# Kernel optimization log

Measured on AMD Instinct MI355X. Metric: run time of the kernel, lower is better.

Reference implementation:

```python
import jax, jax.numpy as jnp
import numpy as np

B, L, D_MODEL, H, D_K, D_V, C = 4, 2048, 512, 8, 64, 64, 5
LN_EPS = 1e-5


def setup_inputs() -> dict:
    key = jax.random.key(0)
    ks = jax.random.split(key, 9)
    u_k = min(int(C * np.log(L)), L)  # 38
    s = 1.0 / np.sqrt(D_MODEL)
    return {
        "input_Q": jax.random.normal(ks[0], (B, L, D_MODEL), jnp.float32),
        "input_K": jax.random.normal(ks[1], (B, L, D_MODEL), jnp.float32),
        "input_V": jax.random.normal(ks[2], (B, L, D_MODEL), jnp.float32),
        "W_Q": jax.random.normal(ks[3], (D_MODEL, H * D_K), jnp.float32) * s,
        "W_K": jax.random.normal(ks[4], (D_MODEL, H * D_K), jnp.float32) * s,
        "W_V": jax.random.normal(ks[5], (D_MODEL, H * D_V), jnp.float32) * s,
        "W_fc": jax.random.normal(ks[6], (H * D_V, D_MODEL), jnp.float32) * (1.0 / np.sqrt(H * D_V)),
        "ln_gamma": jnp.ones((D_MODEL,), jnp.float32),
        "ln_beta": jnp.zeros((D_MODEL,), jnp.float32),
        "index_sample": jax.random.randint(ks[7], (L, u_k), 0, L, jnp.int32),
    }


def reference(input_Q, input_K, input_V, W_Q, W_K, W_V, W_fc, ln_gamma, ln_beta, index_sample):
    Bb, L_Q, _ = input_Q.shape
    L_K = input_K.shape[1]
    u_q = min(int(C * np.log(L_Q)), L_Q)  # n_top queries kept

    # projections -> (B, H, L, d)
    Q = (input_Q @ W_Q).reshape(Bb, L_Q, H, D_K).transpose(0, 2, 1, 3)
    K = (input_K @ W_K).reshape(Bb, L_K, H, D_K).transpose(0, 2, 1, 3)
    V = (input_V @ W_V).reshape(Bb, L_K, H, D_V).transpose(0, 2, 1, 3)

    # sampled QK scores: gather u_k random keys per query position
    K_sample = K[:, :, index_sample, :]                      # (B,H,L_Q,u_k,d_k)
    QK_sample = jnp.einsum('bhqe,bhqke->bhqk', Q, K_sample)  # (B,H,L_Q,u_k)

    # sparsity measure M = max - mean, top-u_q queries
    M = QK_sample.max(axis=-1) - QK_sample.mean(axis=-1)     # (B,H,L_Q)
    _, idx = jax.lax.top_k(M, u_q)                           # (B,H,u_q)

    # attention only for selected queries
    Q_sel = jnp.take_along_axis(Q, idx[..., None], axis=2)   # (B,H,u_q,d_k)
    scores = jnp.einsum('bhue,bhke->bhuk', Q_sel, K) / np.sqrt(D_K)
    attn = jax.nn.softmax(scores, axis=-1)
    values = jnp.einsum('bhuk,bhkd->bhud', attn, V)          # (B,H,u_q,d_v)

    # initial context = mean of V (attn_mask is None), scatter selected rows
    context = jnp.broadcast_to(V.mean(axis=2, keepdims=True), (Bb, H, L_Q, D_V))
    bb = jnp.arange(Bb)[:, None, None]
    hh = jnp.arange(H)[None, :, None]
    context = context.at[bb, hh, idx].set(values)

    context = context.transpose(0, 2, 1, 3).reshape(Bb, L_Q, H * D_V)
    out = context @ W_fc                                     # dropout p=0.0

    y = out + input_Q
    mu = y.mean(axis=-1, keepdims=True)
    var = jnp.mean(jnp.square(y - mu), axis=-1, keepdims=True)
    y = (y - mu) / jnp.sqrt(var + LN_EPS) * ln_gamma + ln_beta
    return y, idx
```

## Files before the change

kernel.cpp:

```cpp
#include <hip/hip_runtime.h>
#include <hip/hip_bf16.h>

#define NB 4
#define NL 2048
#define NH 8
#define NDM 512
#define ND 64
#define KSPLIT 16
#define KTILE 32
#define QB 8

typedef __attribute__((ext_vector_type(8))) short short8b;
typedef __attribute__((ext_vector_type(4))) float f32x4;

__global__ void wconv(const float* __restrict__ W, unsigned short* __restrict__ WT) {
  const int g = blockIdx.x * 256 + threadIdx.x;
  const int k = g >> 9, c = g & 511;
  __hip_bfloat16 hb = __float2bfloat16(W[(size_t)k * 512 + c]);
  WT[(size_t)c * 512 + k] = *reinterpret_cast<unsigned short*>(&hb);
}

__global__ void vmean_colmean(const float* __restrict__ inV, float* __restrict__ parts) {
  const int b = blockIdx.x, seg = blockIdx.y, t = threadIdx.x;
  const float* p = inV + ((size_t)b * NL + seg * 32) * NDM;
  float s0 = 0.f, s1 = 0.f;
  for (int r = 0; r < 32; ++r) {
    s0 += p[(size_t)r * NDM + t];
    s1 += p[(size_t)r * NDM + 256 + t];
  }
  parts[((size_t)b * 64 + seg) * NDM + t] = s0;
  parts[((size_t)b * 64 + seg) * NDM + 256 + t] = s1;
}
__global__ void vmean_gemm(const float* __restrict__ parts, const float* __restrict__ Wv,
                           float* __restrict__ Vm) {
  __shared__ float cm[512];
  const int b = blockIdx.x, t = threadIdx.x;
  float a0 = 0.f, a1 = 0.f;
  for (int g = 0; g < 64; ++g) {
    a0 += parts[((size_t)b * 64 + g) * NDM + t];
    a1 += parts[((size_t)b * 64 + g) * NDM + 256 + t];
  }
  cm[t] = a0 * (1.f / 2048.f);
  cm[t + 256] = a1 * (1.f / 2048.f);
  __syncthreads();
  const int c0 = blockIdx.y * 256 + t;
  float acc = 0.f;
  for (int k = 0; k < 512; ++k) acc += cm[k] * Wv[(size_t)k * NDM + c0];
  Vm[b * 512 + c0] = acc;
}

__global__ __launch_bounds__(256, 4) void proj3(
    const float* __restrict__ AQ, const float* __restrict__ AK,
    const float* __restrict__ wQm, const float* __restrict__ wKm,
    int gh0, float* __restrict__ Qc, float* __restrict__ Kc) {
  __shared__ float As_[32 * 132];
  __shared__ float Ws_[32 * 68];
  const int tid = threadIdx.x;
  const int bm = blockIdx.x;
  const int hl = blockIdx.y;
  const int mat = blockIdx.z;
  const int bh = gh0 + hl;
  const int b = bh >> 3, h = bh & 7;
  const float* A = (mat == 0) ? AQ : AK;
  const float* W = (mat == 0) ? wQm : wKm;
  float* D = (mat == 0) ? Qc : Kc;
  const float* Ab = A + (size_t)b * NL * NDM;
  const int colbase = h * 64;
  const int tm = tid >> 4, tn = tid & 15;
  float acc[8][4] = {};
  for (int k0 = 0; k0 < 512; k0 += 32) {
#pragma unroll
    for (int i = 0; i < 4; ++i) {
      int s = tid + i * 256;
      int r = s >> 3, c4 = (s & 7) * 4;
      float4 v = *reinterpret_cast<const float4*>(Ab + (size_t)(bm * 128 + r) * 512 + k0 + c4);
      As_[(c4 + 0) * 132 + r] = v.x;
      As_[(c4 + 1) * 132 + r] = v.y;
      As_[(c4 + 2) * 132 + r] = v.z;
      As_[(c4 + 3) * 132 + r] = v.w;
    }
#pragma unroll
    for (int i = 0; i < 2; ++i) {
      int s = tid + i * 256;
      int r = s >> 4, c4 = (s & 15) * 4;
      *reinterpret_cast<float4*>(&Ws_[r * 68 + c4]) =
          *reinterpret_cast<const float4*>(W + (size_t)(k0 + r) * 512 + colbase + c4);
    }
    __syncthreads();
#pragma unroll
    for (int kk = 0; kk < 32; ++kk) {
      float4 a0 = *reinterpret_cast<const float4*>(&As_[kk * 132 + tm * 4]);
      float4 a1 = *reinterpret_cast<const float4*>(&As_[kk * 132 + 64 + tm * 4]);
      float4 w  = *reinterpret_cast<const float4*>(&Ws_[kk * 68 + tn * 4]);
      float a[8] = {a0.x, a0.y, a0.z, a0.w, a1.x, a1.y, a1.z, a1.w};
      float wv[4] = {w.x, w.y, w.z, w.w};
#pragma unroll
      for (int ii = 0; ii < 8; ++ii)
#pragma unroll
        for (int jj = 0; jj < 4; ++jj) acc[ii][jj] += a[ii] * wv[jj];
    }
    __syncthreads();
  }
#pragma unroll
  for (int ii = 0; ii < 8; ++ii) {
    int row = bm * 128 + ((ii < 4) ? (tm * 4 + ii) : (64 + tm * 4 + (ii - 4)));
    float4 v = make_float4(acc[ii][0], acc[ii][1], acc[ii][2], acc[ii][3]);
    *reinterpret_cast<float4*>(D + ((size_t)hl * NL + row) * ND + tn * 4) = v;
  }
}

__global__ __launch_bounds__(256) void projV_mfma(
    const float* __restrict__ AV, const unsigned short* __restrict__ WT,
    int gh0, float* __restrict__ Vc) {
  const int wv = threadIdx.x >> 6, l = threadIdx.x & 63;
  const int bm = blockIdx.x;
  const int hl = blockIdx.y;
  const int bh = gh0 + hl;
  const int b = bh >> 3, h = bh & 7;
  const float* Ab = AV + (size_t)b * NL * NDM;
  const int row = bm * 64 + wv * 16 + (l & 15);
  const int kg = (l >> 4) * 8;
  f32x4 acc0 = {}, acc1 = {}, acc2 = {}, acc3 = {};
  for (int k0 = 0; k0 < 512; k0 += 32) {
    const float* ap = Ab + (size_t)row * 512 + k0 + kg;
    float4 v0 = *reinterpret_cast<const float4*>(ap);
    float4 v1 = *reinterpret_cast<const float4*>(ap + 4);
    short8b af;
    {
      __hip_bfloat16 hb;
      hb = __float2bfloat16(v0.x); af[0] = *reinterpret_cast<short*>(&hb);
      hb = __float2bfloat16(v0.y); af[1] = *reinterpret_cast<short*>(&hb);
      hb = __float2bfloat16(v0.z); af[2] = *reinterpret_cast<short*>(&hb);
      hb = __float2bfloat16(v0.w); af[3] = *reinterpret_cast<short*>(&hb);
      hb = __float2bfloat16(v1.x); af[4] = *reinterpret_cast<short*>(&hb);
      hb = __float2bfloat16(v1.y); af[5] = *reinterpret_cast<short*>(&hb);
      hb = __float2bfloat16(v1.z); af[6] = *reinterpret_cast<short*>(&hb);
      hb = __float2bfloat16(v1.w); af[7] = *reinterpret_cast<short*>(&hb);
    }
    const unsigned short* wp = WT + (size_t)(h * 64 + (l & 15)) * 512 + k0 + kg;
    short8b b0 = *reinterpret_cast<const short8b*>(wp);
    short8b b1 = *reinterpret_cast<const short8b*>(wp + 16 * 512);
    short8b b2 = *reinterpret_cast<const short8b*>(wp + 32 * 512);
    short8b b3 = *reinterpret_cast<const short8b*>(wp + 48 * 512);
    acc0 = __builtin_amdgcn_mfma_f32_16x16x32_bf16(af, b0, acc0, 0, 0, 0);
    acc1 = __builtin_amdgcn_mfma_f32_16x16x32_bf16(af, b1, acc1, 0, 0, 0);
    acc2 = __builtin_amdgcn_mfma_f32_16x16x32_bf16(af, b2, acc2, 0, 0, 0);
    acc3 = __builtin_amdgcn_mfma_f32_16x16x32_bf16(af, b3, acc3, 0, 0, 0);
  }
  const int rbase = bm * 64 + wv * 16 + (l >> 4) * 4;
  const int col = l & 15;
#pragma unroll
  for (int j = 0; j < 4; ++j) {
    size_t o = ((size_t)hl * NL + rbase + j) * ND + col;
    Vc[o] = acc0[j];
    Vc[o + 16] = acc1[j];
    Vc[o + 32] = acc2[j];
    Vc[o + 48] = acc3[j];
  }
}

template <int UK>
__global__ __launch_bounds__(256) void sample_scores_t(
    const float* __restrict__ Q, const float* __restrict__ K,
    const int* __restrict__ sampP, float* __restrict__ M) {
  __shared__ float KsAll[4][UK * 66];
  __shared__ float QsAll[4][68];
  const int wv = threadIdx.x >> 6, l = threadIdx.x & 63;
  const int gq = blockIdx.x * 4 + wv;
  const int hl = gq >> 11;
  const int q = gq & 2047;
  float* Ks = KsAll[wv];
  float* Qs = QsAll[wv];
  const float* Kb = K + (size_t)hl * NL * ND;
  Qs[l] = Q[(size_t)gq * ND + l];
  const int base = __builtin_amdgcn_readfirstlane(q) * UK;
#pragma unroll
  for (int r = 0; r < UK; ++r) {
    int kk = sampP[base + r] & (NL - 1);
    Ks[r * 66 + l] = Kb[(size_t)kk * ND + l];
  }
  __syncthreads();
  const int myk = (l < UK) ? l : (UK - 1);
  float acc = 0.f;
#pragma unroll
  for (int j = 0; j < 32; ++j) {
    float2 kv = *reinterpret_cast<const float2*>(&Ks[myk * 66 + 2 * j]);
    float2 qv = *reinterpret_cast<const float2*>(&Qs[2 * j]);
    acc += kv.x * qv.x + kv.y * qv.y;
  }
  float mval = (l < UK) ? acc : -1e30f;
  float sval = (l < UK) ? acc : 0.f;
#pragma unroll
  for (int o = 32; o; o >>= 1) {
    mval = fmaxf(mval, __shfl_xor(mval, o, 64));
    sval += __shfl_xor(sval, o, 64);
  }
  if (l == 0) M[gq] = mval - sval * (1.f / (float)UK);
}

__global__ void sample_scores_gen(const float* __restrict__ Q, const float* __restrict__ K,
                                  const int* __restrict__ sampP, float* __restrict__ M, int uk) {
  const int wave = threadIdx.x >> 6, lane = threadIdx.x & 63;
  const int gq = blockIdx.x * 4 + wave;
  const int hl = gq >> 11;
  const int q = gq & 2047;
  const float qv = Q[(size_t)gq * ND + lane];
  const float* Kbase = K + (size_t)hl * NL * ND;
  float mx = -1e30f, sm = 0.f;
  for (int k = 0; k < uk; ++k) {
    int kidx = sampP[q * uk + k] & (NL - 1);
    float p = qv * Kbase[(size_t)kidx * ND + lane];
#pragma unroll
    for (int o = 32; o; o >>= 1) p += __shfl_xor(p, o, 64);
    mx = fmaxf(mx, p);
    sm += p;
  }
  if (lane == 0) M[gq] = mx - sm / (float)uk;
}

__global__ void topk_kernel(const float* __restrict__ M, int* __restrict__ idxo,
                            float* __restrict__ outIdx, short* __restrict__ selmap,
                            int gh0, int uq) {
  __shared__ float mv[2048];
  __shared__ float bwv[4];
  __shared__ int bwi[4];
  const int bh = blockIdx.x, t = threadIdx.x;
  const int bhg = gh0 + bh;
  const int bb = bhg >> 3, hh = bhg & 7;
  float lv = -1e38f; int li = 1 << 30;
#pragma unroll
  for (int i = 0; i < 8; ++i) {
    int id = t + i * 256;
    float v = M[(size_t)bh * 2048 + id];
    mv[id] = v;
    if (v > lv || (v == lv && id < li)) { lv = v; li = id; }
  }
  __syncthreads();
  for (int it = 0; it < uq; ++it) {
    float bv = lv; int bi = li;
#pragma unroll
    for (int o = 32; o; o >>= 1) {
      float ov = __shfl_xor(bv, o, 64);
      int oi = __shfl_xor(bi, o, 64);
      if (ov > bv || (ov == bv && oi < bi)) { bv = ov; bi = oi; }
    }
    if ((t & 63) == 0) { bwv[t >> 6] = bv; bwi[t >> 6] = bi; }
    __syncthreads();
    float gb = bwv[0]; int gi = bwi[0];
#pragma unroll
    for (int w = 1; w < 4; ++w) {
      if (bwv[w] > gb || (bwv[w] == gb && bwi[w] < gi)) { gb = bwv[w]; gi = bwi[w]; }
    }
    const int sel = gi & (NL - 1);
    if (t == 0) {
      idxo[bh * uq + it] = sel;
      outIdx[bh * uq + it] = (float)sel;
      selmap[((size_t)bb * NL + sel) * NH + hh] = (short)it;
    }
    if ((sel & 255) == t) {
      mv[sel] = -1e38f;
      lv = -1e38f; li = 1 << 30;
#pragma unroll
      for (int i = 0; i < 8; ++i) {
        int id = t + i * 256;
        float v = mv[id];
        if (v > lv || (v == lv && id < li)) { lv = v; li = id; }
      }
    }
    __syncthreads();
  }
}

__global__ __launch_bounds__(256) void attn_part(
    const float* __restrict__ Qw, const float* __restrict__ Kw, const float* __restrict__ Vw,
    const int* __restrict__ idxo, float* __restrict__ pacc, float* __restrict__ pml, int uq) {
  __shared__ float Qs[QB][68];
  __shared__ float Ks[KTILE][68];
  __shared__ float Vs[KTILE][68];
  __shared__ float sc[QB][34];
  const int hl = blockIdx.x, qg = blockIdx.y, ks = blockIdx.z;
  const int t = threadIdx.x;
#pragma unroll
  for (int i = 0; i < 2; ++i) {
    int s = t + i * 256;
    int q = s >> 6, d = s & 63;
    int u = qg * QB + q;
    float v = 0.f;
    if (u < uq) {
      int qi = idxo[hl * uq + u] & (NL - 1);
      v = Qw[((size_t)hl * NL + qi) * ND + d];
    }
    Qs[q][d] = v;
  }
  float m_run = -1e30f, l_run = 0.f;
  float a0 = 0.f, a1 = 0.f;
  const int q2 = t >> 5, ln = t & 31;
  __syncthreads();
  const int kbeg = ks * (NL / KSPLIT);
  for (int k0 = kbeg; k0 < kbeg + NL / KSPLIT; k0 += KTILE) {
#pragma unroll
    for (int i = 0; i < 2; ++i) {
      int s = t + i * 256;
      int r = s >> 4, c4 = (s & 15) * 4;
      *reinterpret_cast<float4*>(&Ks[r][c4]) =
          *reinterpret_cast<const float4*>(Kw + ((size_t)hl * NL + k0 + r) * ND + c4);
      *reinterpret_cast<float4*>(&Vs[r][c4]) =
          *reinterpret_cast<const float4*>(Vw + ((size_t)hl * NL + k0 + r) * ND + c4);
    }
    __syncthreads();
    {
      const int q = t & 7, kk = t >> 3;
      float d0 = 0.f;
#pragma unroll
      for (int dd = 0; dd < 64; dd += 4) {
        float4 qv = *reinterpret_cast<const float4*>(&Qs[q][dd]);
        float4 ka = *reinterpret_cast<const float4*>(&Ks[kk][dd]);
        d0 += qv.x * ka.x + qv.y * ka.y + qv.z * ka.z + qv.w * ka.w;
      }
      sc[q][kk] = d0 * 0.125f;
    }
    __syncthreads();
    {
      float s0 = sc[q2][ln];
      float tmax = s0;
#pragma unroll
      for (int o = 16; o; o >>= 1) tmax = fmaxf(tmax, __shfl_xor(tmax, o, 64));
      float mnew = fmaxf(m_run, tmax);
      float scl = __expf(m_run - mnew);
      float p0 = __expf(s0 - mnew);
      float tsum = p0;
#pragma unroll
      for (int o = 16; o; o >>= 1) tsum += __shfl_xor(tsum, o, 64);
      l_run = l_run * scl + tsum;
      m_run = mnew;
      sc[q2][ln] = p0;
      a0 *= scl; a1 *= scl;
#pragma unroll 8
      for (int k = 0; k < KTILE; ++k) {
        float p = sc[q2][k];
        a0 += p * Vs[k][2 * ln];
        a1 += p * Vs[k][2 * ln + 1];
      }
    }
    __syncthreads();
  }
  const int u = qg * QB + q2;
  if (u < uq) {
    size_t g = ((size_t)hl * uq + u) * KSPLIT + ks;
    pacc[g * ND + 2 * ln] = a0;
    pacc[g * ND + 2 * ln + 1] = a1;
    if (ln == 0) { pml[g * 2] = m_run; pml[g * 2 + 1] = l_run; }
  }
}

__global__ void attn_merge(const float* __restrict__ pacc, const float* __restrict__ pml,
                           float* __restrict__ vals, int uq) {
  const int g = blockIdx.x;
  const int d = threadIdx.x;
  float mstar = -1e30f;
#pragma unroll
  for (int s = 0; s < KSPLIT; ++s) mstar = fmaxf(mstar, pml[((size_t)g * KSPLIT + s) * 2]);
  float num = 0.f, den = 0.f;
#pragma unroll
  for (int s = 0; s < KSPLIT; ++s) {
    float e = __expf(pml[((size_t)g * KSPLIT + s) * 2] - mstar);
    den += e * pml[((size_t)g * KSPLIT + s) * 2 + 1];
    num += e * pacc[((size_t)g * KSPLIT + s) * ND + d];
  }
  vals[(size_t)g * ND + d] = num / den;
}

__global__ void base_gemm(const float* __restrict__ Vm, const float* __restrict__ Wfc,
                          float* __restrict__ base) {
  __shared__ float vm[512];
  const int b = blockIdx.x, t = threadIdx.x;
  vm[t] = Vm[b * 512 + t];
  vm[t + 256] = Vm[b * 512 + t + 256];
  __syncthreads();
  const int c0 = blockIdx.y * 256 + t;
  float acc = 0.f;
  for (int k = 0; k < 512; ++k) acc += vm[k] * Wfc[(size_t)k * 512 + c0];
  base[b * 512 + c0] = acc;
}

__global__ void corr_gemm(const float* __restrict__ vals, const float* __restrict__ Vm,
                          const float* __restrict__ Wfc, float* __restrict__ corr, int uq) {
  __shared__ float diff[64];
  const int g = blockIdx.x, t = threadIdx.x;
  const int bh = g / uq;
  const int h = bh & 7;
  if (t < 64) diff[t] = vals[(size_t)g * 64 + t] - Vm[bh * 64 + t];
  __syncthreads();
  float a0 = 0.f, a1 = 0.f;
#pragma unroll
  for (int d = 0; d < 64; ++d) {
    a0 += diff[d] * Wfc[(size_t)(h * 64 + d) * 512 + t];
    a1 += diff[d] * Wfc[(size_t)(h * 64 + d) * 512 + t + 256];
  }
  corr[(size_t)g * 512 + t] = a0;
  corr[(size_t)g * 512 + t + 256] = a1;
}

__global__ void ln_fused(const float* __restrict__ base, const float* __restrict__ resid,
                         const float* __restrict__ corr, const short* __restrict__ selmap,
                         const float* __restrict__ gamma, const float* __restrict__ beta,
                         float* __restrict__ out, int uq) {
  __shared__ float red[256];
  const int row = blockIdx.x, t = threadIdx.x;
  const int b = row >> 11;
  float y0 = base[b * 512 + t] + resid[(size_t)row * 512 + t];
  float y1 = base[b * 512 + 256 + t] + resid[(size_t)row * 512 + 256 + t];
#pragma unroll
  for (int h = 0; h < NH; ++h) {
    int s = selmap[(size_t)row * NH + h];
    if (s >= 0 && s < uq) {
      const float* cp = corr + (size_t)((b * NH + h) * uq + s) * 512;
      y0 += cp[t];
      y1 += cp[t + 256];
    }
  }
  red[t] = y0 + y1;
  __syncthreads();
  for (int s = 128; s; s >>= 1) { if (t < s) red[t] += red[t + s]; __syncthreads(); }
  const float mu = red[0] * (1.f / 512.f);
  __syncthreads();
  const float d0 = y0 - mu, d1 = y1 - mu;
  red[t] = d0 * d0 + d1 * d1;
  __syncthreads();
  for (int s = 128; s; s >>= 1) { if (t < s) red[t] += red[t + s]; __syncthreads(); }
  const float rs = rsqrtf(red[0] * (1.f / 512.f) + 1e-5f);
  __syncthreads();
  out[(size_t)row * 512 + t] = d0 * rs * gamma[t] + beta[t];
  out[(size_t)row * 512 + 256 + t] = d1 * rs * gamma[256 + t] + beta[256 + t];
}

extern "C" void kernel_launch(void* const* d_in, const int* in_sizes, int n_in,
                              void* d_out, int out_size, void* d_ws, size_t ws_size,
                              hipStream_t stream) {
  const float* inQ = (const float*)d_in[0];
  const float* inK = (const float*)d_in[1];
  const float* inV = (const float*)d_in[2];
  const float* wQ = (const float*)d_in[3];
  const float* wK = (const float*)d_in[4];
  const float* wV = (const float*)d_in[5];
  const float* wFC = (const float*)d_in[6];
  const float* gamma = (const float*)d_in[7];
  const float* beta = (const float*)d_in[8];
  const int* samp = (const int*)d_in[9];

  const int nsamp = in_sizes[9];
  const int uk = nsamp / NL;
  const int uq = uk;
  const int nqg = (uq + QB - 1) / QB;

  if (out_size < NB * NL * NDM + NB * NH * uq) return;

  const size_t perH = 3 * 131072 + 2048 + (size_t)uq * KSPLIT * 64 + (size_t)uq * KSPLIT * 2;
  const size_t fixed = (size_t)32 * uq * 64 + 2048 + 2048 + (size_t)32 * uq * 512
                     + (size_t)32 * uq + 32768 + 131072 + 131072 + 256;
  int hcg = 0;
  for (int c = 32; c >= 1; c >>= 1) {
    if ((perH * (size_t)c + fixed + 256) * 4ull <= ws_size) { hcg = c; break; }
  }
  if (hcg == 0) return;

  float* ws = (float*)d_ws;
  float* Qc = ws;
  float* Kc = Qc + (size_t)hcg * 131072;
  float* Vc = Kc + (size_t)hcg * 131072;
  float* Mb = Vc + (size_t)hcg * 131072;
  float* pacc = Mb + (size_t)hcg * 2048;
  float* pml = pacc + (size_t)hcg * uq * KSPLIT * 64;
  float* vals = pml + (size_t)hcg * uq * KSPLIT * 2;
  float* Vm = vals + (size_t)32 * uq * 64;
  float* base = Vm + 2048;
  float* corr = base + 2048;
  int* idxo = (int*)(corr + (size_t)32 * uq * 512);
  short* selmap = (short*)(idxo + (size_t)32 * uq);
  unsigned short* WTv = (unsigned short*)(selmap + 65536);
  float* vparts = (float*)(WTv + 262144);

  float* out = (float*)d_out;
  float* outIdx = out + (size_t)NB * NL * NDM;

  wconv<<<1024, 256, 0, stream>>>(wV, WTv);
  vmean_colmean<<<dim3(NB, 64), 256, 0, stream>>>(inV, vparts);
  vmean_gemm<<<dim3(NB, 2), 256, 0, stream>>>(vparts, wV, Vm);
  hipMemsetAsync(selmap, 0xFF, (size_t)NB * NL * NH * sizeof(short), stream);

  for (int gh0 = 0; gh0 < NB * NH; gh0 += hcg) {
    proj3<<<dim3(16, hcg, 2), 256, 0, stream>>>(inQ, inK, wQ, wK, gh0, Qc, Kc);
    projV_mfma<<<dim3(32, hcg), 256, 0, stream>>>(inV, WTv, gh0, Vc);
    if (uk == 38)
      sample_scores_t<38><<<hcg * NL / 4, 256, 0, stream>>>(Qc, Kc, samp, Mb);
    else
      sample_scores_gen<<<hcg * NL / 4, 256, 0, stream>>>(Qc, Kc, samp, Mb, uk);
    topk_kernel<<<hcg, 256, 0, stream>>>(Mb, idxo + (size_t)gh0 * uq,
                                         outIdx + (size_t)gh0 * uq, selmap, gh0, uq);
    attn_part<<<dim3(hcg, nqg, KSPLIT), 256, 0, stream>>>(Qc, Kc, Vc,
                                                          idxo + (size_t)gh0 * uq,
                                                          pacc, pml, uq);
    attn_merge<<<hcg * uq, 64, 0, stream>>>(pacc, pml, vals + (size_t)gh0 * uq * ND, uq);
  }

  base_gemm<<<dim3(NB, 2), 256, 0, stream>>>(Vm, wFC, base);
  corr_gemm<<<NB * NH * uq, 256, 0, stream>>>(vals, Vm, wFC, corr, uq);
  ln_fused<<<NB * NL, 256, 0, stream>>>(base, inQ, corr, selmap, gamma, beta, out, uq);
}
```

Measured before the change: 365.2 us.

## Fuse V projection into sample-scores launch and merge attention combine into correction GEMM

The MFMA V projection now runs as extra blocks appended to the sample-scores grid, so the two independent kernels share one launch and can overlap on the GPU. The split-K attention merge is folded into the correction GEMM kernel, which removes one launch per head group and the intermediate vals buffer. Partial accumulators are now sized for all 32 heads so the merge can run once after the loop, which raises workspace use. The V-projection blocks still reserve the sample kernel's static shared memory, which may reduce occupancy.

```diff
diff --git a/kernel.cpp b/kernel.cpp
--- a/kernel.cpp
+++ b/kernel.cpp
@@ -160,9 +160,60 @@
 }
 
 template <int UK>
-__global__ __launch_bounds__(256) void sample_scores_t(
+__global__ __launch_bounds__(256) void sampleV_fused(
     const float* __restrict__ Q, const float* __restrict__ K,
-    const int* __restrict__ sampP, float* __restrict__ M) {
+    const int* __restrict__ sampP, float* __restrict__ M,
+    const float* __restrict__ AV, const unsigned short* __restrict__ WT,
+    int gh0, float* __restrict__ Vc, int nsampBlk) {
+  if ((int)blockIdx.x >= nsampBlk) {
+    const int vblk = blockIdx.x - nsampBlk;
+    const int bm = vblk & 31;
+    const int hl = vblk >> 5;
+    const int wv = threadIdx.x >> 6, l = threadIdx.x & 63;
+    const int bh = gh0 + hl;
+    const int b = bh >> 3, h = bh & 7;
+    const float* Ab = AV + (size_t)b * NL * NDM;
+    const int row = bm * 64 + wv * 16 + (l & 15);
+    const int kg = (l >> 4) * 8;
+    f32x4 acc0 = {}, acc1 = {}, acc2 = {}, acc3 = {};
+    for (int k0 = 0; k0 < 512; k0 += 32) {
+      const float* ap = Ab + (size_t)row * 512 + k0 + kg;
+      float4 v0 = *reinterpret_cast<const float4*>(ap);
+      float4 v1 = *reinterpret_cast<const float4*>(ap + 4);
+      short8b af;
+      {
+        __hip_bfloat16 hb;
+        hb = __float2bfloat16(v0.x); af[0] = *reinterpret_cast<short*>(&hb);
+        hb = __float2bfloat16(v0.y); af[1] = *reinterpret_cast<short*>(&hb);
+        hb = __float2bfloat16(v0.z); af[2] = *reinterpret_cast<short*>(&hb);
+        hb = __float2bfloat16(v0.w); af[3] = *reinterpret_cast<short*>(&hb);
+        hb = __float2bfloat16(v1.x); af[4] = *reinterpret_cast<short*>(&hb);
+        hb = __float2bfloat16(v1.y); af[5] = *reinterpret_cast<short*>(&hb);
+        hb = __float2bfloat16(v1.z); af[6] = *reinterpret_cast<short*>(&hb);
+        hb = __float2bfloat16(v1.w); af[7] = *reinterpret_cast<short*>(&hb);
+      }
+      const unsigned short* wp = WT + (size_t)(h * 64 + (l & 15)) * 512 + k0 + kg;
+      short8b b0 = *reinterpret_cast<const short8b*>(wp);
+      short8b b1 = *reinterpret_cast<const short8b*>(wp + 16 * 512);
+      short8b b2 = *reinterpret_cast<const short8b*>(wp + 32 * 512);
+      short8b b3 = *reinterpret_cast<const short8b*>(wp + 48 * 512);
+      acc0 = __builtin_amdgcn_mfma_f32_16x16x32_bf16(af, b0, acc0, 0, 0, 0);
+      acc1 = __builtin_amdgcn_mfma_f32_16x16x32_bf16(af, b1, acc1, 0, 0, 0);
+      acc2 = __builtin_amdgcn_mfma_f32_16x16x32_bf16(af, b2, acc2, 0, 0, 0);
+      acc3 = __builtin_amdgcn_mfma_f32_16x16x32_bf16(af, b3, acc3, 0, 0, 0);
+    }
+    const int rbase = bm * 64 + wv * 16 + (l >> 4) * 4;
+    const int col = l & 15;
+#pragma unroll
+    for (int j = 0; j < 4; ++j) {
+      size_t o = ((size_t)hl * NL + rbase + j) * ND + col;
+      Vc[o] = acc0[j];
+      Vc[o + 16] = acc1[j];
+      Vc[o + 32] = acc2[j];
+      Vc[o + 48] = acc3[j];
+    }
+    return;
+  }
   __shared__ float KsAll[4][UK * 66];
   __shared__ float QsAll[4][68];
   const int wv = threadIdx.x >> 6, l = threadIdx.x & 63;
@@ -353,21 +404,35 @@
   }
 }
 
-__global__ void attn_merge(const float* __restrict__ pacc, const float* __restrict__ pml,
-                           float* __restrict__ vals, int uq) {
-  const int g = blockIdx.x;
-  const int d = threadIdx.x;
-  float mstar = -1e30f;
-#pragma unroll
-  for (int s = 0; s < KSPLIT; ++s) mstar = fmaxf(mstar, pml[((size_t)g * KSPLIT + s) * 2]);
-  float num = 0.f, den = 0.f;
-#pragma unroll
-  for (int s = 0; s < KSPLIT; ++s) {
-    float e = __expf(pml[((size_t)g * KSPLIT + s) * 2] - mstar);
-    den += e * pml[((size_t)g * KSPLIT + s) * 2 + 1];
-    num += e * pacc[((size_t)g * KSPLIT + s) * ND + d];
-  }
-  vals[(size_t)g * ND + d] = num / den;
+__global__ void corr_merge(const float* __restrict__ pacc, const float* __restrict__ pml,
+                           const float* __restrict__ Vm, const float* __restrict__ Wfc,
+                           float* __restrict__ corr, int uq) {
+  __shared__ float diff[64];
+  const int g = blockIdx.x, t = threadIdx.x;
+  const int bh = g / uq;
+  const int h = bh & 7;
+  if (t < 64) {
+    float mstar = -1e30f;
+#pragma unroll
+    for (int s = 0; s < KSPLIT; ++s) mstar = fmaxf(mstar, pml[((size_t)g * KSPLIT + s) * 2]);
+    float num = 0.f, den = 0.f;
+#pragma unroll
+    for (int s = 0; s < KSPLIT; ++s) {
+      float e = __expf(pml[((size_t)g * KSPLIT + s) * 2] - mstar);
+      den += e * pml[((size_t)g * KSPLIT + s) * 2 + 1];
+      num += e * pacc[((size_t)g * KSPLIT + s) * ND + t];
+    }
+    diff[t] = num / den - Vm[(size_t)bh * 64 + t];
+  }
+  __syncthreads();
+  float a0 = 0.f, a1 = 0.f;
+#pragma unroll
+  for (int d = 0; d < 64; ++d) {
+    a0 += diff[d] * Wfc[(size_t)(h * 64 + d) * 512 + t];
+    a1 += diff[d] * Wfc[(size_t)(h * 64 + d) * 512 + t + 256];
+  }
+  corr[(size_t)g * 512 + t] = a0;
+  corr[(size_t)g * 512 + t + 256] = a1;
 }
 
 __global__ void base_gemm(const float* __restrict__ Vm, const float* __restrict__ Wfc,
@@ -381,24 +446,6 @@
   float acc = 0.f;
   for (int k = 0; k < 512; ++k) acc += vm[k] * Wfc[(size_t)k * 512 + c0];
   base[b * 512 + c0] = acc;
-}
-
-__global__ void corr_gemm(const float* __restrict__ vals, const float* __restrict__ Vm,
-                          const float* __restrict__ Wfc, float* __restrict__ corr, int uq) {
-  __shared__ float diff[64];
-  const int g = blockIdx.x, t = threadIdx.x;
-  const int bh = g / uq;
-  const int h = bh & 7;
-  if (t < 64) diff[t] = vals[(size_t)g * 64 + t] - Vm[bh * 64 + t];
-  __syncthreads();
-  float a0 = 0.f, a1 = 0.f;
-#pragma unroll
-  for (int d = 0; d < 64; ++d) {
-    a0 += diff[d] * Wfc[(size_t)(h * 64 + d) * 512 + t];
-    a1 += diff[d] * Wfc[(size_t)(h * 64 + d) * 512 + t + 256];
-  }
-  corr[(size_t)g * 512 + t] = a0;
-  corr[(size_t)g * 512 + t + 256] = a1;
 }
 
 __global__ void ln_fused(const float* __restrict__ base, const float* __restrict__ resid,
@@ -455,9 +502,10 @@
 
   if (out_size < NB * NL * NDM + NB * NH * uq) return;
 
-  const size_t perH = 3 * 131072 + 2048 + (size_t)uq * KSPLIT * 64 + (size_t)uq * KSPLIT * 2;
-  const size_t fixed = (size_t)32 * uq * 64 + 2048 + 2048 + (size_t)32 * uq * 512
-                     + (size_t)32 * uq + 32768 + 131072 + 131072 + 256;
+  const size_t perH = 3 * 131072 + 2048;
+  const size_t fixed = (size_t)32 * uq * KSPLIT * 64 + (size_t)32 * uq * KSPLIT * 2
+                     + 2048 + 2048 + (size_t)32 * uq * 512 + (size_t)32 * uq
+                     + 32768 + 131072 + 131072 + 256;
   int hcg = 0;
   for (int c = 32; c >= 1; c >>= 1) {
     if ((perH * (size_t)c + fixed + 256) * 4ull <= ws_size) { hcg = c; break; }
@@ -470,9 +518,8 @@
   float* Vc = Kc + (size_t)hcg * 131072;
   float* Mb = Vc + (size_t)hcg * 131072;
   float* pacc = Mb + (size_t)hcg * 2048;
-  float* pml = pacc + (size_t)hcg * uq * KSPLIT * 64;
-  float* vals = pml + (size_t)hcg * uq * KSPLIT * 2;
-  float* Vm = vals + (size_t)32 * uq * 64;
+  float* pml = pacc + (size_t)32 * uq * KSPLIT * 64;
+  float* Vm = pml + (size_t)32 * uq * KSPLIT * 2;
   float* base = Vm + 2048;
   float* corr = base + 2048;
   int* idxo = (int*)(corr + (size_t)32 * uq * 512);
@@ -490,20 +537,23 @@
 
   for (int gh0 = 0; gh0 < NB * NH; gh0 += hcg) {
     proj3<<<dim3(16, hcg, 2), 256, 0, stream>>>(inQ, inK, wQ, wK, gh0, Qc, Kc);
-    projV_mfma<<<dim3(32, hcg), 256, 0, stream>>>(inV, WTv, gh0, Vc);
-    if (uk == 38)
-      sample_scores_t<38><<<hcg * NL / 4, 256, 0, stream>>>(Qc, Kc, samp, Mb);
-    else
+    if (uk == 38) {
+      const int nsampBlk = hcg * NL / 4;
+      sampleV_fused<38><<<nsampBlk + hcg * 32, 256, 0, stream>>>(
+          Qc, Kc, samp, Mb, inV, WTv, gh0, Vc, nsampBlk);
+    } else {
+      projV_mfma<<<dim3(32, hcg), 256, 0, stream>>>(inV, WTv, gh0, Vc);
       sample_scores_gen<<<hcg * NL / 4, 256, 0, stream>>>(Qc, Kc, samp, Mb, uk);
+    }
     topk_kernel<<<hcg, 256, 0, stream>>>(Mb, idxo + (size_t)gh0 * uq,
                                          outIdx + (size_t)gh0 * uq, selmap, gh0, uq);
-    attn_part<<<dim3(hcg, nqg, KSPLIT), 256, 0, stream>>>(Qc, Kc, Vc,
-                                                          idxo + (size_t)gh0 * uq,
-                                                          pacc, pml, uq);
-    attn_merge<<<hcg * uq, 64, 0, stream>>>(pacc, pml, vals + (size_t)gh0 * uq * ND, uq);
+    attn_part<<<dim3(hcg, nqg, KSPLIT), 256, 0, stream>>>(
+        Qc, Kc, Vc, idxo + (size_t)gh0 * uq,
+        pacc + (size_t)gh0 * uq * KSPLIT * 64,
+        pml + (size_t)gh0 * uq * KSPLIT * 2, uq);
   }
 
   base_gemm<<<dim3(NB, 2), 256, 0, stream>>>(Vm, wFC, base);
-  corr_gemm<<<NB * NH * uq, 256, 0, stream>>>(vals, Vm, wFC, corr, uq);
+  corr_merge<<<NB * NH * uq, 256, 0, stream>>>(pacc, pml, Vm, wFC, corr, uq);
   ln_fused<<<NB * NL, 256, 0, stream>>>(base, inQ, corr, selmap, gamma, beta, out, uq);
 }
```

Result: no change. 365.5 us (+0.1%).
